# Kernel tuning notes

Hardware: AMD Instinct MI355X
Metric: run time of the kernel (lower is better)

## Reference

```python
import jax, jax.numpy as jnp
import numpy as np

NEG = jnp.finfo(jnp.float32).min


def setup_inputs() -> dict:
    key = jax.random.key(0)
    k1, k2, k3 = jax.random.split(key, 3)
    B, H, S, D = 1, 12, 4096, 64
    query = jax.random.normal(k1, (B, H, S, D), dtype=jnp.float32)
    key_t = jax.random.normal(k2, (B, H, S, D), dtype=jnp.float32)
    value = jax.random.normal(k3, (B, H, S, D), dtype=jnp.float32)
    attention_mask = jnp.ones((B, S), dtype=jnp.int32)  # 2D mask -> causal branch
    return {
        "query": query,
        "key": key_t,
        "value": value,
        "attention_mask": attention_mask,
        "sliding_window": 128,
    }


def reference(query, key, value, attention_mask, sliding_window):
    # query/key/value: [B, H, S, D]
    B, H, S, D = query.shape
    scaling = 1.0 / jnp.sqrt(jnp.float32(D))
    # QK^T scaled: [B, H, S, S]
    attn_weights = jnp.einsum("bhqd,bhkd->bhqk", query, key) * scaling
    i = jnp.arange(S)[:, None]
    j = jnp.arange(S)[None, :]
    # 2D attention_mask branch: causal triu mask (values of mask not used)
    causal_mask = jnp.where(j > i, NEG, 0.0).astype(attn_weights.dtype)
    attn_weights = attn_weights + causal_mask
    # sliding window: row i allows columns [max(0, i - sw + 1), i]
    sw_allowed = (j >= i - sliding_window + 1) & (j <= i)
    sw_mask = jnp.where(sw_allowed, 0.0, NEG).astype(jnp.float32)
    attn_weights = attn_weights + sw_mask[None, None, :, :]
    # softmax in float32, cast back to query dtype
    attn_weights = jax.nn.softmax(attn_weights.astype(jnp.float32), axis=-1).astype(query.dtype)
    # probs @ V, then transpose heads: [B, S, H, D]
    attn_output = jnp.einsum("bhqk,bhkd->bhqd", attn_weights, value)
    attn_output = jnp.transpose(attn_output, (0, 2, 1, 3))
    return attn_output, attn_weights
```

## Files before the change

### kernel.cpp

```cpp
#include <hip/hip_runtime.h>
#include <math.h>

#define NH 12
#define SEQ 4096
#define DIM 64
#define SW 128
#define RPB 16
#define TPB 256
#define KSTRIDE 65
#define MAXK (RPB + SW - 1)

typedef float v4f __attribute__((ext_vector_type(4)));

__global__ __launch_bounds__(256)
void zero_fill_kernel(v4f* __restrict__ dst, size_t n4) {
    const size_t stride = (size_t)gridDim.x * blockDim.x;
    const v4f z = {0.f, 0.f, 0.f, 0.f};
    for (size_t i = (size_t)blockIdx.x * blockDim.x + threadIdx.x; i < n4; i += stride) {
        __builtin_nontemporal_store(z, dst + i);
    }
}

__global__ __launch_bounds__(TPB, 2)
void attn_band_kernel(const float* __restrict__ Q, const float* __restrict__ K,
                      const float* __restrict__ V, float* __restrict__ Wout,
                      float* __restrict__ Oout) {
    __shared__ float KV[MAXK * KSTRIDE];
    __shared__ float Qs[RPB * DIM];
    __shared__ float Ps[RPB * SW];

    const int h    = blockIdx.x / (SEQ / RPB);
    const int tile = blockIdx.x % (SEQ / RPB);
    const int r0   = tile * RPB;
    const int kLo  = max(0, r0 - (SW - 1));
    const int kHi  = r0 + RPB - 1;
    const int nK   = kHi - kLo + 1;

    const float* Qh = Q + (size_t)h * SEQ * DIM;
    const float* Kh = K + (size_t)h * SEQ * DIM;
    const float* Vh = V + (size_t)h * SEQ * DIM;

    const int tid = threadIdx.x;

    for (int idx = tid; idx < nK * (DIM / 4); idx += TPB) {
        const int row = idx >> 4;
        const int c4  = (idx & 15) * 4;
        const float4 v = *(const float4*)(Kh + (size_t)(kLo + row) * DIM + c4);
        float* dst = &KV[row * KSTRIDE + c4];
        dst[0] = v.x; dst[1] = v.y; dst[2] = v.z; dst[3] = v.w;
    }
    for (int idx = tid; idx < RPB * (DIM / 4); idx += TPB) {
        const int row = idx >> 4;
        const int c4  = (idx & 15) * 4;
        *(float4*)&Qs[row * DIM + c4] =
            *(const float4*)(Qh + (size_t)(r0 + row) * DIM + c4);
    }
    __syncthreads();

    const int wave = tid >> 6;
    const int lane = tid & 63;
    const float scale = 0.125f;

    for (int t = 0; t < 4; ++t) {
        const int r  = wave * 4 + t;
        const int i  = r0 + r;
        const int w0 = max(0, i - (SW - 1));

        float s0 = -INFINITY, s1 = -INFINITY;
        {
            const int col = w0 + lane;
            if (col <= i) {
                const float* kr = &KV[(col - kLo) * KSTRIDE];
                const float* qr = &Qs[r * DIM];
                float acc = 0.f;
                #pragma unroll
                for (int d = 0; d < DIM; ++d) acc += qr[d] * kr[d];
                s0 = acc * scale;
            }
        }
        {
            const int col = w0 + 64 + lane;
            if (col <= i) {
                const float* kr = &KV[(col - kLo) * KSTRIDE];
                const float* qr = &Qs[r * DIM];
                float acc = 0.f;
                #pragma unroll
                for (int d = 0; d < DIM; ++d) acc += qr[d] * kr[d];
                s1 = acc * scale;
            }
        }
        float m = fmaxf(s0, s1);
        #pragma unroll
        for (int o = 32; o > 0; o >>= 1) m = fmaxf(m, __shfl_xor(m, o, 64));
        const float e0 = __expf(s0 - m);
        const float e1 = __expf(s1 - m);
        float sum = e0 + e1;
        #pragma unroll
        for (int o = 32; o > 0; o >>= 1) sum += __shfl_xor(sum, o, 64);
        const float inv = 1.0f / sum;
        Ps[r * SW + lane]      = e0 * inv;
        Ps[r * SW + 64 + lane] = e1 * inv;
    }
    __syncthreads();

    for (int idx = tid; idx < nK * (DIM / 4); idx += TPB) {
        const int row = idx >> 4;
        const int c4  = (idx & 15) * 4;
        *(float4*)&KV[row * DIM + c4] =
            *(const float4*)(Vh + (size_t)(kLo + row) * DIM + c4);
    }
    __syncthreads();

    {
        const int rbase = wave * 4;
        const int i0 = r0 + rbase;
        const int u0 = max(0, i0 - (SW - 1));
        const int u1 = i0 + 3;

        float acc0 = 0.f, acc1 = 0.f, acc2 = 0.f, acc3 = 0.f;
        for (int j = u0; j <= u1; ++j) {
            const float v = KV[(j - kLo) * DIM + lane];
            {   const int i = i0 + 0, w0 = max(0, i - (SW - 1)), rel = j - w0;
                if (rel >= 0 && j <= i) acc0 += Ps[(rbase + 0) * SW + rel] * v; }
            {   const int i = i0 + 1, w0 = max(0, i - (SW - 1)), rel = j - w0;
                if (rel >= 0 && j <= i) acc1 += Ps[(rbase + 1) * SW + rel] * v; }
            {   const int i = i0 + 2, w0 = max(0, i - (SW - 1)), rel = j - w0;
                if (rel >= 0 && j <= i) acc2 += Ps[(rbase + 2) * SW + rel] * v; }
            {   const int i = i0 + 3, w0 = max(0, i - (SW - 1)), rel = j - w0;
                if (rel >= 0 && j <= i) acc3 += Ps[(rbase + 3) * SW + rel] * v; }
        }
        Oout[((size_t)(i0 + 0) * NH + h) * DIM + lane] = acc0;
        Oout[((size_t)(i0 + 1) * NH + h) * DIM + lane] = acc1;
        Oout[((size_t)(i0 + 2) * NH + h) * DIM + lane] = acc2;
        Oout[((size_t)(i0 + 3) * NH + h) * DIM + lane] = acc3;

        #pragma unroll
        for (int t = 0; t < 4; ++t) {
            const int r  = rbase + t;
            const int i  = r0 + r;
            const int w0 = max(0, i - (SW - 1));
            const int cstart = w0 >> 2;
            const int cend   = i >> 2;
            const int c = cstart + lane;
            if (c <= cend) {
                const int col0 = c * 4;
                float vv[4];
                #pragma unroll
                for (int k = 0; k < 4; ++k) {
                    const int col = col0 + k;
                    const int rel = min(max(col - w0, 0), SW - 1);
                    const float p = Ps[r * SW + rel];
                    vv[k] = (col >= w0 && col <= i) ? p : 0.f;
                }
                float* wrow = Wout + ((size_t)(h * SEQ + i)) * SEQ;
                *(float4*)(wrow + col0) = make_float4(vv[0], vv[1], vv[2], vv[3]);
            }
        }
    }
}

extern "C" void kernel_launch(void* const* d_in, const int* in_sizes, int n_in,
                              void* d_out, int out_size, void* d_ws, size_t ws_size,
                              hipStream_t stream) {
    const float* Q = (const float*)d_in[0];
    const float* K = (const float*)d_in[1];
    const float* V = (const float*)d_in[2];

    float* Oout = (float*)d_out;
    float* Wout = (float*)d_out + (size_t)SEQ * NH * DIM;

    const size_t n4 = (size_t)NH * SEQ * SEQ / 4;
    zero_fill_kernel<<<4096, 256, 0, stream>>>((v4f*)Wout, n4);

    dim3 grid(NH * (SEQ / RPB));
    attn_band_kernel<<<grid, TPB, 0, stream>>>(Q, K, V, Wout, Oout);
}
```

Before: 1.050 ms.

## Fuse zero-fill into band kernel and skip zeroing band chunks

Merges the separate zero-fill kernel into the attention kernel by adding extra blocks that zero only the float4 chunks outside each row's sliding-window band. The band blocks write the band chunks, so the two regions no longer overlap and ordering between them does not matter. This removes a kernel launch and the redundant writes to band chunks, and lets the fill overlap with the band compute. In exchange, the fill loop does per-chunk index math and uses plain stores instead of nontemporal stores, and the launch-bounds occupancy hint of 2 is dropped.

```diff
diff --git a/kernel.cpp b/kernel.cpp
--- a/kernel.cpp
+++ b/kernel.cpp
@@ -9,25 +9,34 @@
 #define TPB 256
 #define KSTRIDE 65
 #define MAXK (RPB + SW - 1)
+#define BAND_BLOCKS (NH * (SEQ / RPB))
+#define FILL_BLOCKS 8192
+#define NCHUNK ((size_t)NH * SEQ * (SEQ / 4))
 
-typedef float v4f __attribute__((ext_vector_type(4)));
-
-__global__ __launch_bounds__(256)
-void zero_fill_kernel(v4f* __restrict__ dst, size_t n4) {
-    const size_t stride = (size_t)gridDim.x * blockDim.x;
-    const v4f z = {0.f, 0.f, 0.f, 0.f};
-    for (size_t i = (size_t)blockIdx.x * blockDim.x + threadIdx.x; i < n4; i += stride) {
-        __builtin_nontemporal_store(z, dst + i);
-    }
-}
-
-__global__ __launch_bounds__(TPB, 2)
-void attn_band_kernel(const float* __restrict__ Q, const float* __restrict__ K,
-                      const float* __restrict__ V, float* __restrict__ Wout,
-                      float* __restrict__ Oout) {
+__global__ __launch_bounds__(TPB)
+void attn_fused_kernel(const float* __restrict__ Q, const float* __restrict__ K,
+                       const float* __restrict__ V, float* __restrict__ Wout,
+                       float* __restrict__ Oout) {
     __shared__ float KV[MAXK * KSTRIDE];
     __shared__ float Qs[RPB * DIM];
     __shared__ float Ps[RPB * SW];
+
+    if (blockIdx.x >= BAND_BLOCKS) {
+        const size_t tid0   = (size_t)(blockIdx.x - BAND_BLOCKS) * TPB + threadIdx.x;
+        const size_t stride = (size_t)FILL_BLOCKS * TPB;
+        const float4 z = make_float4(0.f, 0.f, 0.f, 0.f);
+        for (size_t idx = tid0; idx < NCHUNK; idx += stride) {
+            const int ci = (int)(idx & 1023);
+            const int i  = (int)((idx >> 10) & 4095);
+            const int w0 = max(0, i - (SW - 1));
+            const int cstart = w0 >> 2;
+            const int cend   = i >> 2;
+            if (ci < cstart || ci > cend) {
+                *(float4*)((float*)Wout + idx * 4) = z;
+            }
+        }
+        return;
+    }
 
     const int h    = blockIdx.x / (SEQ / RPB);
     const int tile = blockIdx.x % (SEQ / RPB);
@@ -169,9 +178,6 @@
     float* Oout = (float*)d_out;
     float* Wout = (float*)d_out + (size_t)SEQ * NH * DIM;
 
-    const size_t n4 = (size_t)NH * SEQ * SEQ / 4;
-    zero_fill_kernel<<<4096, 256, 0, stream>>>((v4f*)Wout, n4);
-
-    dim3 grid(NH * (SEQ / RPB));
-    attn_band_kernel<<<grid, TPB, 0, stream>>>(Q, K, V, Wout, Oout);
+    dim3 grid(BAND_BLOCKS + FILL_BLOCKS);
+    attn_fused_kernel<<<grid, TPB, 0, stream>>>(Q, K, V, Wout, Oout);
 }
```

Measured after the change: 1.019 ms. 1.03x faster.
